# Optimization experiments

Measured on AMD Instinct MI355X. Metric: run time of the kernel, lower is better.

## Reference

```python
import jax, jax.numpy as jnp
import numpy as np

LAMBDA_CM = 0.5
LAMBDA_DIV = 0.1
EPS = 1e-8


def _normalize(x):
    # F.normalize(dim=-1): x / max(||x||, 1e-12)
    n = jnp.linalg.norm(x, axis=-1, keepdims=True)
    return x / jnp.maximum(n, 1e-12)


def _cdist(z, c):
    # Euclidean pairwise distance [N, K], matching torch.cdist(p=2)
    d2 = (jnp.sum(z * z, axis=-1, keepdims=True)
          + jnp.sum(c * c, axis=-1)[None, :]
          - 2.0 * (z @ c.T))
    return jnp.sqrt(jnp.maximum(d2, 0.0))


def setup_inputs() -> dict:
    key = jax.random.key(0)
    ks = jax.random.split(key, 7)
    N, dim_a, dim_b, embed_dim, n_codes = 8192, 1024, 1024, 512, 4096
    a = jax.random.normal(ks[0], (N, dim_a), dtype=jnp.float32)
    b = jax.random.normal(ks[1], (N, dim_b), dtype=jnp.float32)
    # Linear params (kaiming-uniform-ish scale)
    Wa = jax.random.uniform(ks[2], (embed_dim, dim_a), jnp.float32, -1, 1) / np.sqrt(dim_a)
    ba = jnp.zeros((embed_dim,), jnp.float32)
    Wb = jax.random.uniform(ks[3], (embed_dim, dim_b), jnp.float32, -1, 1) / np.sqrt(dim_b)
    bb = jnp.zeros((embed_dim,), jnp.float32)
    # Orthogonal-init codebook [n_codes, embed_dim] (n_codes > embed_dim -> orthonormal columns)
    g = jax.random.normal(ks[4], (n_codes, embed_dim), dtype=jnp.float32)
    q, _ = jnp.linalg.qr(g)
    codebook = q[:, :embed_dim] if q.shape[1] >= embed_dim else g / np.sqrt(embed_dim)
    codebook = jnp.asarray(codebook, jnp.float32)
    return {"a": a, "b": b, "Wa": Wa, "ba": ba, "Wb": Wb, "bb": bb, "codebook": codebook}


def reference(a, b, Wa, ba, Wb, bb, codebook):
    sg = jax.lax.stop_gradient
    za = _normalize(a @ Wa.T + ba)  # [N, D]
    zb = _normalize(b @ Wb.T + bb)  # [N, D]

    da = _cdist(za, codebook)       # [N, K]
    db = _cdist(zb, codebook)       # [N, K]
    idx_a = jnp.argmin(da, axis=-1)
    idx_b = jnp.argmin(db, axis=-1)
    qa = codebook[idx_a]            # [N, D]
    qb = codebook[idx_b]

    mse = lambda x, y: jnp.mean((x - y) ** 2)
    rec = (mse(qa, sg(za)) + mse(qb, sg(zb))
           + 0.25 * (mse(za, sg(qa)) + mse(zb, sg(qb))))

    sim = (za @ zb.T) / 0.07        # [N, N]
    N = sim.shape[0]
    diag = jnp.arange(N)
    ce_ab = -jnp.mean(jax.nn.log_softmax(sim, axis=-1)[diag, diag])
    ce_ba = -jnp.mean(jax.nn.log_softmax(sim.T, axis=-1)[diag, diag])
    cm = (ce_ab + ce_ba) / 2

    avg_a = jnp.mean(jax.nn.softmax(-da * 5.0, axis=-1), axis=0)  # [K]
    avg_b = jnp.mean(jax.nn.softmax(-db * 5.0, axis=-1), axis=0)
    div = (-(avg_a * jnp.log(avg_a + EPS)).sum()
           - (avg_b * jnp.log(avg_b + EPS)).sum()) / 2

    loss = rec + LAMBDA_CM * cm - LAMBDA_DIV * div
    match = jnp.mean((idx_a == idx_b).astype(jnp.float32))
    return loss, match
```

## Files before the change

kernel.cpp:

```cpp
#include <hip/hip_runtime.h>
#include <hip/hip_bf16.h>
#include <math.h>
#include <float.h>

typedef __attribute__((ext_vector_type(8))) short s8bf;
typedef __attribute__((ext_vector_type(4))) float f32x4;

typedef const __attribute__((address_space(1))) void g_void;
typedef __attribute__((address_space(3))) void lds_void;

__device__ inline ushort f2bf(float x) {
    unsigned int u = __float_as_uint(x);
    unsigned int r = (u + 0x7FFFu + ((u >> 16) & 1u)) >> 16;
    return (ushort)r;
}
__device__ inline ushort f2bf_fast(float x) {
    return (ushort)((__float_as_uint(x) + 0x8000u) >> 16);
}
__device__ inline float2 bf2x2(unsigned int u) {
    float2 r;
    r.x = __uint_as_float(u << 16);
    r.y = __uint_as_float(u & 0xFFFF0000u);
    return r;
}

__global__ __launch_bounds__(256) void k_cvt_bf16(
    const float* __restrict__ src, ushort* __restrict__ dst, size_t n)
{
    size_t i = ((size_t)blockIdx.x * 256 + threadIdx.x) * 4;
    size_t stride = (size_t)gridDim.x * 256 * 4;
    for (; i < n; i += stride) {
        float4 v = *(const float4*)(src + i);
        ushort4 o;
        o.x = f2bf(v.x); o.y = f2bf(v.y); o.z = f2bf(v.z); o.w = f2bf(v.w);
        *(ushort4*)(dst + i) = o;
    }
}

__device__ inline const ushort* stage_ptr(const ushort* M, size_t ld, int ra, int tid)
{
    const int row  = tid >> 2;
    const int slot = tid & 3;
    const int scol = ((slot ^ ((row >> 1) & 3)) << 3);
    return M + (size_t)(ra + row) * ld + scol;
}

__device__ inline void stage_issue2(const ushort* pa, const ushort* pb,
                                    size_t off64a, size_t off64b,
                                    ushort* As, ushort* Bs, int tid)
{
    const int wb = (tid >> 6) << 9;
    __builtin_amdgcn_global_load_lds((g_void*)pa,            (lds_void*)(As + wb),        16, 0, 0);
    __builtin_amdgcn_global_load_lds((g_void*)(pa + off64a), (lds_void*)(As + 2048 + wb), 16, 0, 0);
    __builtin_amdgcn_global_load_lds((g_void*)pb,            (lds_void*)(Bs + wb),        16, 0, 0);
    __builtin_amdgcn_global_load_lds((g_void*)(pb + off64b), (lds_void*)(Bs + 2048 + wb), 16, 0, 0);
}

__device__ inline void mma_tile(const ushort* As, const ushort* Bs,
                                int wr, int wc, int lane, f32x4 acc[4][4])
{
    const int hi = lane >> 4, lo = lane & 15;
    const int soff = ((hi ^ ((lo >> 1) & 3)) << 3);
    s8bf af[4], bfr[4];
#pragma unroll
    for (int m = 0; m < 4; ++m)
        af[m] = *(const s8bf*)(As + (wr * 64 + m * 16 + lo) * 32 + soff);
#pragma unroll
    for (int n = 0; n < 4; ++n)
        bfr[n] = *(const s8bf*)(Bs + (wc * 64 + n * 16 + lo) * 32 + soff);
#pragma unroll
    for (int m = 0; m < 4; ++m)
#pragma unroll
        for (int n = 0; n < 4; ++n)
            acc[m][n] = __builtin_amdgcn_mfma_f32_16x16x32_bf16(
                af[m], bfr[n], acc[m][n], 0, 0, 0);
}

#define DBUF_DECL  __shared__ __align__(16) ushort Lds[2][8192]
#define AS(p) (&Lds[p][0])
#define BS(p) (&Lds[p][4096])

__global__ __launch_bounds__(256) void k_mfma_gemm_bias2(
    const ushort* __restrict__ Aa, const ushort* __restrict__ Wa,
    const float* __restrict__ ba, float* __restrict__ Ca,
    const ushort* __restrict__ Ab, const ushort* __restrict__ Wb,
    const float* __restrict__ bb, float* __restrict__ Cb,
    int Ncols, int Kd)
{
    DBUF_DECL;
    const int z = blockIdx.z;
    const ushort* A = z ? Ab : Aa;
    const ushort* W = z ? Wb : Wa;
    const float* bias = z ? bb : ba;
    float* C = z ? Cb : Ca;

    const int tid = threadIdx.x, lane = tid & 63, wid = tid >> 6;
    const int wr = wid >> 1, wc = wid & 1;
    const int rbase = blockIdx.x * 128, cbase = blockIdx.y * 128;
    const int hi = lane >> 4, lo = lane & 15;
    const int KS = Kd >> 5;
    const size_t o64 = (size_t)64 * Kd;

    f32x4 acc[4][4];
#pragma unroll
    for (int m = 0; m < 4; ++m)
#pragma unroll
        for (int n = 0; n < 4; ++n)
#pragma unroll
            for (int j = 0; j < 4; ++j) acc[m][n][j] = 0.f;

    const ushort* pa = stage_ptr(A, Kd, rbase, tid);
    const ushort* pb = stage_ptr(W, Kd, cbase, tid);
    stage_issue2(pa, pb, o64, o64, AS(0), BS(0), tid);
    __syncthreads();
    int phase = 0;
    for (int ks = 0; ks < KS; ++ks) {
        pa += 32; pb += 32;
        if (ks + 1 < KS)
            stage_issue2(pa, pb, o64, o64, AS(phase ^ 1), BS(phase ^ 1), tid);
        mma_tile(AS(phase), BS(phase), wr, wc, lane, acc);
        __syncthreads();
        phase ^= 1;
    }
#pragma unroll
    for (int n = 0; n < 4; ++n) {
        int col = cbase + wc * 64 + n * 16 + lo;
        float bv = bias[col];
#pragma unroll
        for (int m = 0; m < 4; ++m)
#pragma unroll
            for (int j = 0; j < 4; ++j) {
                int row = rbase + wr * 64 + m * 16 + hi * 4 + j;
                C[(size_t)row * Ncols + col] = acc[m][n][j] + bv;
            }
    }
}

__global__ __launch_bounds__(256) void k_normalize2(
    const float* __restrict__ Za, ushort* __restrict__ Zab,
    const float* __restrict__ Zb, ushort* __restrict__ Zbb, int N, int D)
{
    const float* Z = blockIdx.y ? Zb : Za;
    ushort* Zo = blockIdx.y ? Zbb : Zab;
    const int lane = threadIdx.x & 63, wid = threadIdx.x >> 6;
    const int row = blockIdx.x * 4 + wid;
    if (row >= N) return;
    const float4* p = (const float4*)(Z + (size_t)row * D);
    const int nf4 = D >> 2;
    float ss = 0.f;
    for (int f = lane; f < nf4; f += 64) {
        float4 v = p[f];
        ss += v.x * v.x + v.y * v.y + v.z * v.z + v.w * v.w;
    }
#pragma unroll
    for (int msk = 1; msk < 64; msk <<= 1) ss += __shfl_xor(ss, msk, 64);
    float sc = 1.0f / fmaxf(sqrtf(ss), 1e-12f);
    ushort4* pb = (ushort4*)(Zo + (size_t)row * D);
    for (int f = lane; f < nf4; f += 64) {
        float4 v = p[f];
        ushort4 u;
        u.x = f2bf(v.x * sc); u.y = f2bf(v.y * sc);
        u.z = f2bf(v.z * sc); u.w = f2bf(v.w * sc);
        pb[f] = u;
    }
}

__global__ __launch_bounds__(256) void k_rownorm2(
    const float* __restrict__ X, float* __restrict__ out, int N, int D)
{
    const int lane = threadIdx.x & 63, wid = threadIdx.x >> 6;
    const int row = blockIdx.x * 4 + wid;
    if (row >= N) return;
    const float4* p = (const float4*)(X + (size_t)row * D);
    const int nf4 = D >> 2;
    float ss = 0.f;
    for (int f = lane; f < nf4; f += 64) {
        float4 v = p[f];
        ss += v.x * v.x + v.y * v.y + v.z * v.z + v.w * v.w;
    }
#pragma unroll
    for (int msk = 1; msk < 64; msk <<= 1) ss += __shfl_xor(ss, msk, 64);
    if (lane == 0) out[row] = ss;
}

#define EIGHT_PROLOG(XPTR, YPTR)                                               \
    const int tid = threadIdx.x, lane = tid & 63, wid = tid >> 6;              \
    const int wr = wid >> 2, wc = wid & 3;                                     \
    const int hi = lane >> 4, lo = lane & 15;                                  \
    const int fsw = ((hi ^ ((lo >> 1) & 3)) << 3);                             \
    const int KT = D >> 5, KTm = KT - 1;                                       \
    const int NIT = (chunkCols >> 8) << 5 >> 1; \
    const size_t o128 = (size_t)128 * D;                                       \
    const ushort* pa = stage_ptr(XPTR, D, rbase, tid);                         \
    const ushort* pb = stage_ptr(YPTR, D, c0, tid);

__device__ inline void issue8(ushort* Lbuf, const ushort* qa, const ushort* qb,
                              size_t o128, int wid)
{
    ushort* A0 = Lbuf + (wid << 9);
    ushort* B0 = Lbuf + 8192 + (wid << 9);
    __builtin_amdgcn_global_load_lds((g_void*)qa,          (lds_void*)A0,          16, 0, 0);
    __builtin_amdgcn_global_load_lds((g_void*)(qa + o128), (lds_void*)(A0 + 4096), 16, 0, 0);
    __builtin_amdgcn_global_load_lds((g_void*)qb,          (lds_void*)B0,          16, 0, 0);
    __builtin_amdgcn_global_load_lds((g_void*)(qb + o128), (lds_void*)(B0 + 4096), 16, 0, 0);
}

__global__ __launch_bounds__(512, 2) void k_sim8(
    const ushort* __restrict__ X, const ushort* __restrict__ Y,
    float* __restrict__ pl, float* __restrict__ colsum,
    int Ntot, int D, int chunkCols)
{
    __shared__ __align__(16) ushort L3[3][16384];
    const int rbase = blockIdx.x * 256;
    const int c0 = blockIdx.y * chunkCols;
    const float inv_t = 1.0f / 0.07f;
    EIGHT_PROLOG(X, Y)

    f32x4 acc[8][4];
    float Ls[32];
#pragma unroll
    for (int m = 0; m < 8; ++m)
#pragma unroll
        for (int n = 0; n < 4; ++n)
#pragma unroll
            for (int j = 0; j < 4; ++j) acc[m][n][j] = 0.f;
#pragma unroll
    for (int i = 0; i < 32; ++i) Ls[i] = 0.f;

    issue8(&L3[0][0], pa, pb, o128, wid);
    pa += 32; pb += 32;
    issue8(&L3[1][0], pa, pb, o128, wid);
    if ((1 & KTm) == KTm) { pa -= (D - 32); pb += (size_t)256 * D - (D - 32); }
    else { pa += 32; pb += 32; }

    int ibuf = 0, sbuf = 2, kk = 0, tcol = 0;
    for (int it = 0; it < NIT; ++it) {
        const int s = it + 2;
        if (s < NIT) {
            issue8(&L3[sbuf][0], pa, pb, o128, wid);
            if ((s & KTm) == KTm) { pa -= (D - 32); pb += (size_t)256 * D - (D - 32); }
            else { pa += 32; pb += 32; }
            if (++sbuf == 3) sbuf = 0;
            asm volatile("s_waitcnt vmcnt(8)" ::: "memory");
        } else if (it + 1 < NIT) {
            asm volatile("s_waitcnt vmcnt(4)" ::: "memory");
        } else {
            asm volatile("s_waitcnt vmcnt(0)" ::: "memory");
        }
        __builtin_amdgcn_sched_barrier(0);
        __builtin_amdgcn_s_barrier();

        const ushort* Ab = &L3[ibuf][0];
        const ushort* Bb = &L3[ibuf][8192];
        s8bf bfr[4];
#pragma unroll
        for (int n = 0; n < 4; ++n)
            bfr[n] = *(const s8bf*)(Bb + (wc * 64 + n * 16 + lo) * 32 + fsw);
        __builtin_amdgcn_s_setprio(1);
#pragma unroll
        for (int m = 0; m < 4; ++m) {
            s8bf a = *(const s8bf*)(Ab + (wr * 128 + m * 16 + lo) * 32 + fsw);
#pragma unroll
            for (int n = 0; n < 4; ++n)
                acc[m][n] = __builtin_amdgcn_mfma_f32_16x16x32_bf16(a, bfr[n], acc[m][n], 0, 0, 0);
        }
        __builtin_amdgcn_s_setprio(0);
        __builtin_amdgcn_s_barrier();
        __builtin_amdgcn_s_setprio(1);
#pragma unroll
        for (int m = 4; m < 8; ++m) {
            s8bf a = *(const s8bf*)(Ab + (wr * 128 + m * 16 + lo) * 32 + fsw);
#pragma unroll
            for (int n = 0; n < 4; ++n)
                acc[m][n] = __builtin_amdgcn_mfma_f32_16x16x32_bf16(a, bfr[n], acc[m][n], 0, 0, 0);
        }
        __builtin_amdgcn_s_setprio(0);
        __builtin_amdgcn_s_barrier();
        if (++ibuf == 3) ibuf = 0;

        if (++kk == KT) {
            kk = 0;
            const int cbase = c0 + tcol * 256 + wc * 64;
            float csum[4] = {0.f, 0.f, 0.f, 0.f};
#pragma unroll
            for (int m = 0; m < 8; ++m)
#pragma unroll
                for (int j = 0; j < 4; ++j) {
                    const int i = m * 4 + j;
#pragma unroll
                    for (int n = 0; n < 4; ++n) {
                        float e = __expf(acc[m][n][j] * inv_t);
                        Ls[i] += e;
                        csum[n] += e;
                        acc[m][n][j] = 0.f;
                    }
                }
#pragma unroll
            for (int n = 0; n < 4; ++n) {
                float cs = csum[n];
                cs += __shfl_xor(cs, 16, 64);
                cs += __shfl_xor(cs, 32, 64);
                if (hi == 0) atomicAdd(&colsum[cbase + n * 16 + lo], cs);
            }
            ++tcol;
        }
    }
#pragma unroll
    for (int i = 0; i < 32; ++i) {
#pragma unroll
        for (int msk = 1; msk < 16; msk <<= 1)
            Ls[i] += __shfl_xor(Ls[i], msk, 64);
    }
    if (lo == 0) {
        const int slot = blockIdx.y * 4 + wc;
#pragma unroll
        for (int m = 0; m < 8; ++m)
#pragma unroll
            for (int j = 0; j < 4; ++j) {
                int row = rbase + wr * 128 + m * 16 + hi * 4 + j;
                pl[(size_t)slot * Ntot + row] = Ls[m * 4 + j];
            }
    }
}

__global__ __launch_bounds__(512, 2) void k_dist8(
    const ushort* __restrict__ Za, const ushort* __restrict__ Zb,
    const ushort* __restrict__ CB, const float* __restrict__ cn,
    ushort* __restrict__ expm_a, ushort* __restrict__ expm_b,
    int Ntot, int Ktot, int D, int chunkCols)
{
    __shared__ __align__(16) ushort L3[3][16384];
    const ushort* Z = blockIdx.z ? Zb : Za;
    ushort* expm = blockIdx.z ? expm_b : expm_a;
    const int rbase = blockIdx.x * 256;
    const int c0 = blockIdx.y * chunkCols;
    EIGHT_PROLOG(Z, CB)

    f32x4 acc[8][4];
#pragma unroll
    for (int m = 0; m < 8; ++m)
#pragma unroll
        for (int n = 0; n < 4; ++n)
#pragma unroll
            for (int j = 0; j < 4; ++j) acc[m][n][j] = 0.f;

    issue8(&L3[0][0], pa, pb, o128, wid);
    pa += 32; pb += 32;
    issue8(&L3[1][0], pa, pb, o128, wid);
    if ((1 & KTm) == KTm) { pa -= (D - 32); pb += (size_t)256 * D - (D - 32); }
    else { pa += 32; pb += 32; }

    int ibuf = 0, sbuf = 2, kk = 0, tcol = 0;
    for (int it = 0; it < NIT; ++it) {
        const int s = it + 2;
        if (s < NIT) {
            issue8(&L3[sbuf][0], pa, pb, o128, wid);
            if ((s & KTm) == KTm) { pa -= (D - 32); pb += (size_t)256 * D - (D - 32); }
            else { pa += 32; pb += 32; }
            if (++sbuf == 3) sbuf = 0;
            asm volatile("s_waitcnt vmcnt(8)" ::: "memory");
        } else if (it + 1 < NIT) {
            asm volatile("s_waitcnt vmcnt(4)" ::: "memory");
        } else {
            asm volatile("s_waitcnt vmcnt(0)" ::: "memory");
        }
        __builtin_amdgcn_sched_barrier(0);
        __builtin_amdgcn_s_barrier();

        const ushort* Ab = &L3[ibuf][0];
        const ushort* Bb = &L3[ibuf][8192];
        s8bf bfr[4];
#pragma unroll
        for (int n = 0; n < 4; ++n)
            bfr[n] = *(const s8bf*)(Bb + (wc * 64 + n * 16 + lo) * 32 + fsw);
        __builtin_amdgcn_s_setprio(1);
#pragma unroll
        for (int m = 0; m < 4; ++m) {
            s8bf a = *(const s8bf*)(Ab + (wr * 128 + m * 16 + lo) * 32 + fsw);
#pragma unroll
            for (int n = 0; n < 4; ++n)
                acc[m][n] = __builtin_amdgcn_mfma_f32_16x16x32_bf16(a, bfr[n], acc[m][n], 0, 0, 0);
        }
        __builtin_amdgcn_s_setprio(0);
        __builtin_amdgcn_s_barrier();
        __builtin_amdgcn_s_setprio(1);
#pragma unroll
        for (int m = 4; m < 8; ++m) {
            s8bf a = *(const s8bf*)(Ab + (wr * 128 + m * 16 + lo) * 32 + fsw);
#pragma unroll
            for (int n = 0; n < 4; ++n)
                acc[m][n] = __builtin_amdgcn_mfma_f32_16x16x32_bf16(a, bfr[n], acc[m][n], 0, 0, 0);
        }
        __builtin_amdgcn_s_setprio(0);
        __builtin_amdgcn_s_barrier();
        if (++ibuf == 3) ibuf = 0;

        if (++kk == KT) {
            kk = 0;
            const int cbase = c0 + tcol * 256 + wc * 64;
            float cnv[4];
#pragma unroll
            for (int n = 0; n < 4; ++n) cnv[n] = 1.0f + cn[cbase + n * 16 + lo];
#pragma unroll
            for (int m = 0; m < 8; ++m)
#pragma unroll
                for (int j = 0; j < 4; ++j) {
                    const int row = rbase + wr * 128 + m * 16 + hi * 4 + j;
                    ushort* erow = expm + (size_t)row * Ktot + cbase + lo;
#pragma unroll
                    for (int n = 0; n < 4; ++n) {
                        float d = sqrtf(fmaxf(cnv[n] - 2.0f * acc[m][n][j], 0.f));
                        erow[n * 16] = f2bf_fast(__expf(-5.0f * d));
                        acc[m][n][j] = 0.f;
                    }
                }
            ++tcol;
        }
    }
}

__global__ __launch_bounds__(256) void k_row_stats(
    const ushort* __restrict__ expm_a, const ushort* __restrict__ expm_b,
    int* __restrict__ idx_a, float* __restrict__ lse_a, float* __restrict__ inv_a,
    int* __restrict__ idx_b, float* __restrict__ lse_b, float* __restrict__ inv_b,
    int Ktot)
{
    const int z = blockIdx.y;
    const ushort* expm = z ? expm_b : expm_a;
    int* idx = z ? idx_b : idx_a;
    float* lse = z ? lse_b : lse_a;
    float* inv = z ? inv_b : inv_a;
    const int lane = threadIdx.x & 63, wid = threadIdx.x >> 6;
    const int row = blockIdx.x * 4 + wid;
    const uint4* p = (const uint4*)(expm + (size_t)row * Ktot);
    const int nf8 = Ktot >> 3;
    float s = 0.f, best = -1.f;
    int bk = 0;
    for (int f = lane; f < nf8; f += 64) {
        uint4 u = p[f];
        const unsigned* w = (const unsigned*)&u;
        const int k0 = f << 3;
#pragma unroll
        for (int q = 0; q < 4; ++q) {
            float2 e = bf2x2(w[q]);
            s += e.x + e.y;
            if (e.x > best) { best = e.x; bk = k0 + 2 * q; }
            if (e.y > best) { best = e.y; bk = k0 + 2 * q + 1; }
        }
    }
#pragma unroll
    for (int msk = 1; msk < 64; msk <<= 1) {
        float ob = __shfl_xor(best, msk, 64);
        int   ok = __shfl_xor(bk, msk, 64);
        s += __shfl_xor(s, msk, 64);
        if (ob > best || (ob == best && ok < bk)) { best = ob; bk = ok; }
    }
    if (lane == 0) {
        idx[row] = bk;
        lse[row] = __logf(s);
        inv[row] = 1.0f / s;
    }
}

__global__ __launch_bounds__(256) void k_avg_stream(
    const ushort* __restrict__ expm_a, const ushort* __restrict__ expm_b,
    const float* __restrict__ inv_a, const float* __restrict__ inv_b,
    float* __restrict__ avg_a, float* __restrict__ avg_b,
    int Ktot, int rows)
{
    const int z = blockIdx.z;
    const ushort* expm = z ? expm_b : expm_a;
    const float* invL = z ? inv_b : inv_a;
    float* avg = z ? avg_b : avg_a;
    const int c = blockIdx.x * 1024 + threadIdx.x * 4;
    const int r0 = blockIdx.y * rows;
    float4 s = {0.f, 0.f, 0.f, 0.f};
    for (int r = r0; r < r0 + rows; ++r) {
        float il = invL[r];
        uint2 u = *(const uint2*)(expm + (size_t)r * Ktot + c);
        float2 e0 = bf2x2(u.x);
        float2 e1 = bf2x2(u.y);
        s.x = fmaf(e0.x, il, s.x);
        s.y = fmaf(e0.y, il, s.y);
        s.z = fmaf(e1.x, il, s.z);
        s.w = fmaf(e1.y, il, s.w);
    }
    atomicAdd(&avg[c + 0], s.x);
    atomicAdd(&avg[c + 1], s.y);
    atomicAdd(&avg[c + 2], s.z);
    atomicAdd(&avg[c + 3], s.w);
}

__global__ __launch_bounds__(256) void k_mfma_dist1_noexp(
    const ushort* __restrict__ Za, const ushort* __restrict__ Zb,
    const ushort* __restrict__ CB,
    const float* __restrict__ cn, float* __restrict__ pd,
    float* __restrict__ pls, int* __restrict__ pib,
    int Ntot, int D, int chunkCols)
{
    DBUF_DECL;
    const int z = blockIdx.z;
    const ushort* Z = z ? Zb : Za;
    const int tid = threadIdx.x, lane = tid & 63, wid = tid >> 6;
    const int wr = wid >> 1, wc = wid & 1;
    const int rbase = blockIdx.x * 128;
    const int c0 = blockIdx.y * chunkCols;
    const int hi = lane >> 4, lo = lane & 15;
    const int KS = D >> 5, TILES = chunkCols >> 7;
    const size_t o64 = (size_t)64 * D;
    const ptrdiff_t dWrapA = -(ptrdiff_t)(D - 32);
    const ptrdiff_t dWrapB = (ptrdiff_t)128 * D - (ptrdiff_t)(D - 32);

    float bd[16], ls[16]; int bi[16];
#pragma unroll
    for (int i = 0; i < 16; ++i) { bd[i] = FLT_MAX; ls[i] = 0.f; bi[i] = 0; }

    const ushort* pa = stage_ptr(Z, D, rbase, tid);
    const ushort* pb = stage_ptr(CB, D, c0, tid);
    stage_issue2(pa, pb, o64, o64, AS(0), BS(0), tid);
    __syncthreads();
    int phase = 0;
    for (int t = 0; t < TILES; ++t) {
        f32x4 acc[4][4];
#pragma unroll
        for (int m = 0; m < 4; ++m)
#pragma unroll
            for (int n = 0; n < 4; ++n)
#pragma unroll
                for (int j = 0; j < 4; ++j) acc[m][n][j] = 0.f;
        for (int ks = 0; ks < KS; ++ks) {
            const bool wrap = (ks + 1 == KS);
            pa += wrap ? dWrapA : 32;
            pb += wrap ? dWrapB : 32;
            if (!(wrap && t + 1 == TILES))
                stage_issue2(pa, pb, o64, o64, AS(phase ^ 1), BS(phase ^ 1), tid);
            mma_tile(AS(phase), BS(phase), wr, wc, lane, acc);
            __syncthreads();
            phase ^= 1;
        }
        const int cbase = c0 + (t << 7) + wc * 64;
        float cnv[4]; int cix[4];
#pragma unroll
        for (int n = 0; n < 4; ++n) {
            cix[n] = cbase + n * 16 + lo;
            cnv[n] = cn[cix[n]];
        }
#pragma unroll
        for (int m = 0; m < 4; ++m)
#pragma unroll
            for (int j = 0; j < 4; ++j) {
                const int i = m * 4 + j;
#pragma unroll
                for (int n = 0; n < 4; ++n) {
                    float d = sqrtf(fmaxf(1.0f + cnv[n] - 2.0f * acc[m][n][j], 0.f));
                    if (d < bd[i]) { bd[i] = d; bi[i] = cix[n]; }
                    ls[i] += __expf(-5.0f * d);
                }
            }
    }
#pragma unroll
    for (int i = 0; i < 16; ++i) {
#pragma unroll
        for (int msk = 1; msk < 16; msk <<= 1) {
            float od = __shfl_xor(bd[i], msk, 64);
            int   oi = __shfl_xor(bi[i], msk, 64);
            ls[i] += __shfl_xor(ls[i], msk, 64);
            if (od < bd[i] || (od == bd[i] && oi < bi[i])) { bd[i] = od; bi[i] = oi; }
        }
    }
    if (lo == 0) {
        const int slot = (z * gridDim.y + blockIdx.y) * 2 + wc;
#pragma unroll
        for (int m = 0; m < 4; ++m)
#pragma unroll
            for (int j = 0; j < 4; ++j) {
                int row = rbase + wr * 64 + m * 16 + hi * 4 + j;
                pd [(size_t)slot * Ntot + row] = bd[m * 4 + j];
                pls[(size_t)slot * Ntot + row] = ls[m * 4 + j];
                pib[(size_t)slot * Ntot + row] = bi[m * 4 + j];
            }
    }
}

__global__ __launch_bounds__(256) void k_dist1_reduce2(
    const float* __restrict__ pd, const float* __restrict__ pls,
    const int* __restrict__ pib,
    int* __restrict__ idx_a, float* __restrict__ lse_a, float* __restrict__ inv_a,
    int* __restrict__ idx_b, float* __restrict__ lse_b, float* __restrict__ inv_b,
    int Ntot, int slots)
{
    const int z = blockIdx.y;
    int row = blockIdx.x * 256 + threadIdx.x;
    if (row >= Ntot) return;
    const float* pdz = pd + (size_t)z * slots * Ntot;
    const float* plz = pls + (size_t)z * slots * Ntot;
    const int*   piz = pib + (size_t)z * slots * Ntot;
    float bd = FLT_MAX; int bi = 0;
    float L = 0.f;
    for (int s = 0; s < slots; ++s) {
        float d = pdz[(size_t)s * Ntot + row];
        int   i = piz[(size_t)s * Ntot + row];
        if (d < bd || (d == bd && i < bi)) { bd = d; bi = i; }
        L += plz[(size_t)s * Ntot + row];
    }
    if (z) { idx_b[row] = bi; lse_b[row] = __logf(L); inv_b[row] = 1.0f / L; }
    else   { idx_a[row] = bi; lse_a[row] = __logf(L); inv_a[row] = 1.0f / L; }
}

__global__ __launch_bounds__(256) void k_mfma_dist2(
    const ushort* __restrict__ Za, const ushort* __restrict__ Zb,
    const ushort* __restrict__ CB, const float* __restrict__ cn,
    const float* __restrict__ lse_a, const float* __restrict__ lse_b,
    float* __restrict__ avg_a, float* __restrict__ avg_b,
    int Ntot, int D, int chunkCols)
{
    DBUF_DECL;
    const ushort* Z = blockIdx.z ? Zb : Za;
    const float* lse = blockIdx.z ? lse_b : lse_a;
    float* avg = blockIdx.z ? avg_b : avg_a;
    const int tid = threadIdx.x, lane = tid & 63, wid = tid >> 6;
    const int wr = wid >> 1, wc = wid & 1;
    const int rbase = blockIdx.x * 128;
    const int c0 = blockIdx.y * chunkCols;
    const int hi = lane >> 4, lo = lane & 15;
    const int KS = D >> 5, TILES = chunkCols >> 7;
    const size_t o64 = (size_t)64 * D;
    const ptrdiff_t dWrapA = -(ptrdiff_t)(D - 32);
    const ptrdiff_t dWrapB = (ptrdiff_t)128 * D - (ptrdiff_t)(D - 32);

    float lr[16];
#pragma unroll
    for (int m = 0; m < 4; ++m)
#pragma unroll
        for (int j = 0; j < 4; ++j)
            lr[m * 4 + j] = lse[rbase + wr * 64 + m * 16 + hi * 4 + j];

    const ushort* pa = stage_ptr(Z, D, rbase, tid);
    const ushort* pb = stage_ptr(CB, D, c0, tid);
    stage_issue2(pa, pb, o64, o64, AS(0), BS(0), tid);
    __syncthreads();
    int phase = 0;
    for (int t = 0; t < TILES; ++t) {
        f32x4 acc[4][4];
#pragma unroll
        for (int m = 0; m < 4; ++m)
#pragma unroll
            for (int n = 0; n < 4; ++n)
#pragma unroll
                for (int j = 0; j < 4; ++j) acc[m][n][j] = 0.f;
        for (int ks = 0; ks < KS; ++ks) {
            const bool wrap = (ks + 1 == KS);
            pa += wrap ? dWrapA : 32;
            pb += wrap ? dWrapB : 32;
            if (!(wrap && t + 1 == TILES))
                stage_issue2(pa, pb, o64, o64, AS(phase ^ 1), BS(phase ^ 1), tid);
            mma_tile(AS(phase), BS(phase), wr, wc, lane, acc);
            __syncthreads();
            phase ^= 1;
        }
        const int cbase = c0 + (t << 7) + wc * 64;
        float cnv[4];
#pragma unroll
        for (int n = 0; n < 4; ++n) cnv[n] = cn[cbase + n * 16 + lo];
        float colsum[4] = {0.f, 0.f, 0.f, 0.f};
#pragma unroll
        for (int m = 0; m < 4; ++m)
#pragma unroll
            for (int j = 0; j < 4; ++j) {
                const int i = m * 4 + j;
#pragma unroll
                for (int n = 0; n < 4; ++n) {
                    float d = sqrtf(fmaxf(1.0f + cnv[n] - 2.0f * acc[m][n][j], 0.f));
                    colsum[n] += __expf(-5.0f * d - lr[i]);
                }
            }
#pragma unroll
        for (int n = 0; n < 4; ++n) {
            float cs = colsum[n];
            cs += __shfl_xor(cs, 16, 64);
            cs += __shfl_xor(cs, 32, 64);
            if (hi == 0) atomicAdd(&avg[cbase + n * 16 + lo], cs);
        }
    }
}

__global__ __launch_bounds__(256) void k_sum_log_reduce(
    const float* __restrict__ pl, float* __restrict__ out, int Ntot, int slots)
{
    int row = blockIdx.x * 256 + threadIdx.x;
    if (row >= Ntot) return;
    float L = 0.f;
    for (int s = 0; s < slots; ++s)
        L += pl[(size_t)s * Ntot + row];
    out[row] = __logf(L);
}

__global__ __launch_bounds__(256) void k_log_inplace(
    const float* __restrict__ src, float* __restrict__ dst, int n)
{
    int i = blockIdx.x * 256 + threadIdx.x;
    if (i < n) dst[i] = __logf(src[i]);
}

__global__ __launch_bounds__(256) void k_rec_match(
    const ushort* __restrict__ za, const ushort* __restrict__ zb,
    const ushort* __restrict__ cbk,
    const int* __restrict__ idx_a, const int* __restrict__ idx_b,
    const float* __restrict__ lse_ab, const float* __restrict__ lse_ba,
    float* __restrict__ acc, int N, int D)
{
    const int tid = threadIdx.x, lane = tid & 63, wid = tid >> 6;
    const int gw = blockIdx.x * 4 + wid;
    const int nw = gridDim.x * 4;
    const int nf8 = D >> 3;
    float pa = 0.f, pb = 0.f, pdot = 0.f;
    for (int row = gw; row < N; row += nw) {
        const int ia = idx_a[row], ib = idx_b[row];
        const uint4* pza = (const uint4*)(za + (size_t)row * D);
        const uint4* pzb = (const uint4*)(zb + (size_t)row * D);
        const uint4* pca = (const uint4*)(cbk + (size_t)ia * D);
        const uint4* pcb = (const uint4*)(cbk + (size_t)ib * D);
        for (int f = lane; f < nf8; f += 64) {
            uint4 ua = pza[f], ub = pzb[f], uc = pca[f], ud = pcb[f];
            const unsigned int* wa = (const unsigned int*)&ua;
            const unsigned int* wb = (const unsigned int*)&ub;
            const unsigned int* wc2 = (const unsigned int*)&uc;
            const unsigned int* wd = (const unsigned int*)&ud;
#pragma unroll
            for (int q = 0; q < 4; ++q) {
                float2 va = bf2x2(wa[q]), vb = bf2x2(wb[q]);
                float2 ca = bf2x2(wc2[q]), cb = bf2x2(wd[q]);
                float dx = va.x - ca.x, dy = va.y - ca.y;
                pa += dx * dx + dy * dy;
                dx = vb.x - cb.x; dy = vb.y - cb.y;
                pb += dx * dx + dy * dy;
                pdot += va.x * vb.x + va.y * vb.y;
            }
        }
    }
    float slab = 0.f, slba = 0.f, smatch = 0.f;
    for (int r = blockIdx.x * 256 + tid; r < N; r += gridDim.x * 256) {
        slab += lse_ab[r];
        slba += lse_ba[r];
        if (idx_a[r] == idx_b[r]) smatch += 1.f;
    }
#pragma unroll
    for (int msk = 1; msk < 64; msk <<= 1) {
        pa += __shfl_xor(pa, msk, 64);
        pb += __shfl_xor(pb, msk, 64);
        pdot += __shfl_xor(pdot, msk, 64);
        slab += __shfl_xor(slab, msk, 64);
        slba += __shfl_xor(slba, msk, 64);
        smatch += __shfl_xor(smatch, msk, 64);
    }
    __shared__ float red[4][6];
    if (lane == 0) {
        red[wid][0] = pa; red[wid][1] = pb; red[wid][2] = slab;
        red[wid][3] = slba; red[wid][4] = smatch; red[wid][5] = pdot;
    }
    __syncthreads();
    if (tid < 6) {
        float s = red[0][tid] + red[1][tid] + red[2][tid] + red[3][tid];
        atomicAdd(&acc[tid], s);
    }
}

__global__ __launch_bounds__(256) void k_finalize(
    const float* __restrict__ avg_a, const float* __restrict__ avg_b,
    const float* __restrict__ acc, float* __restrict__ out,
    int N, int D, int K)
{
    __shared__ float red[256];
    const int tid = threadIdx.x;
    const float invN = 1.0f / (float)N;
    float sa = 0.f, sb = 0.f;
    for (int k = tid; k < K; k += 256) {
        float va = avg_a[k] * invN;
        float vb = avg_b[k] * invN;
        sa += va * logf(va + 1e-8f);
        sb += vb * logf(vb + 1e-8f);
    }
    red[tid] = sa;
    __syncthreads();
    for (int s = 128; s > 0; s >>= 1) {
        if (tid < s) red[tid] += red[tid + s];
        __syncthreads();
    }
    float entA = -red[0];
    __syncthreads();
    red[tid] = sb;
    __syncthreads();
    for (int s = 128; s > 0; s >>= 1) {
        if (tid < s) red[tid] += red[tid + s];
        __syncthreads();
    }
    if (tid == 0) {
        float entB = -red[0];
        float nd = (float)N * (float)D;
        float rec = 1.25f * (acc[0] / nd + acc[1] / nd);
        float sdot = acc[5] / 0.07f;
        float cm  = 0.5f * ((acc[2] - sdot) + (acc[3] - sdot)) * invN;
        float div = 0.5f * (entA + entB);
        out[0] = rec + 0.5f * cm - 0.1f * div;
        out[1] = acc[4] * invN;
    }
}

extern "C" void kernel_launch(void* const* d_in, const int* in_sizes, int n_in,
                              void* d_out, int out_size, void* d_ws, size_t ws_size,
                              hipStream_t stream)
{
    const float* a   = (const float*)d_in[0];
    const float* b   = (const float*)d_in[1];
    const float* Wa  = (const float*)d_in[2];
    const float* ba  = (const float*)d_in[3];
    const float* Wb  = (const float*)d_in[4];
    const float* bb  = (const float*)d_in[5];
    const float* cbk = (const float*)d_in[6];

    const int D  = in_sizes[3];
    const int dA = in_sizes[2] / D;
    const int dB = in_sizes[4] / D;
    const int N  = in_sizes[0] / dA;
    const int K  = in_sizes[6] / D;

    char* w = (char*)d_ws;
    size_t off = 0;
    auto alloc = [&](size_t bytes) -> void* {
        void* p = w + off;
        off = (off + bytes + 255) & ~(size_t)255;
        return p;
    };
    float*  za     = (float*)alloc((size_t)N * D * 4);
    float*  zb     = (float*)alloc((size_t)N * D * 4);
    float*  cn     = (float*)alloc((size_t)K * 4);
    int*    idx_a  = (int*)  alloc((size_t)N * 4);
    int*    idx_b  = (int*)  alloc((size_t)N * 4);
    float*  lse_a  = (float*)alloc((size_t)N * 4);
    float*  lse_b  = (float*)alloc((size_t)N * 4);
    float*  inv_a  = (float*)alloc((size_t)N * 4);
    float*  inv_b  = (float*)alloc((size_t)N * 4);
    float*  lse_ab = (float*)alloc((size_t)N * 4);
    float*  lse_ba = (float*)alloc((size_t)N * 4);
    float*  avgreg = (float*)alloc(((size_t)2 * K + 8) * 4);
    float*  avg_a  = avgreg;
    float*  avg_b  = avgreg + K;
    float*  accb   = avgreg + 2 * K;
    ushort* Wa_bf  = (ushort*)alloc((size_t)D * dA * 2);
    ushort* Wb_bf  = (ushort*)alloc((size_t)D * dB * 2);
    ushort* cbk_bf = (ushort*)alloc((size_t)K * D * 2);
    ushort* regionA = (ushort*)alloc((size_t)N * dA * 2);
    ushort* a_bf  = regionA;
    ushort* za_bf = regionA;
    ushort* zb_bf = regionA + (size_t)N * D;
    ushort* regionB = (ushort*)alloc((size_t)N * dB * 2);
    ushort* b_bf   = regionB;
    float* pl     = (float*)regionB;
    float* pd     = pl  + (size_t)32 * N;
    float* pls    = pd  + (size_t)64 * N;
    int*   pib    = (int*)(pls + (size_t)64 * N);
    float* colsum = (float*)(pib + (size_t)64 * N);
    if (off > ws_size) return;
    ushort* expm_a = (ushort*)alloc((size_t)N * K * 2);
    ushort* expm_b = (ushort*)alloc((size_t)N * K * 2);
    const bool useExp = (off <= ws_size);

    dim3 blk(256);
    dim3 blk8(512);

    k_cvt_bf16<<<1024, blk, 0, stream>>>(a,   a_bf,   (size_t)N * dA);
    k_cvt_bf16<<<1024, blk, 0, stream>>>(b,   b_bf,   (size_t)N * dB);
    k_cvt_bf16<<<256,  blk, 0, stream>>>(Wa,  Wa_bf,  (size_t)D * dA);
    k_cvt_bf16<<<256,  blk, 0, stream>>>(Wb,  Wb_bf,  (size_t)D * dB);
    k_cvt_bf16<<<512,  blk, 0, stream>>>(cbk, cbk_bf, (size_t)K * D);

    k_mfma_gemm_bias2<<<dim3(N / 128, D / 128, 2), blk, 0, stream>>>(
        a_bf, Wa_bf, ba, za, b_bf, Wb_bf, bb, zb, D, dA);

    k_normalize2<<<dim3((N + 3) / 4, 2), blk, 0, stream>>>(za, za_bf, zb, zb_bf, N, D);
    k_rownorm2<<<dim3((K + 3) / 4), blk, 0, stream>>>(cbk, cn, K, D);
    hipMemsetAsync(avgreg, 0, ((size_t)2 * K + 8) * 4, stream);
    hipMemsetAsync(colsum, 0, (size_t)N * 4, stream);

    if (useExp) {
        const int dchunk = 1024;
        k_dist8<<<dim3(N / 256, K / dchunk, 2), blk8, 0, stream>>>(
            za_bf, zb_bf, cbk_bf, cn, expm_a, expm_b, N, K, D, dchunk);
        k_row_stats<<<dim3(N / 4, 2), blk, 0, stream>>>(
            expm_a, expm_b, idx_a, lse_a, inv_a, idx_b, lse_b, inv_b, K);
        k_avg_stream<<<dim3(K / 1024, N / 64, 2), blk, 0, stream>>>(
            expm_a, expm_b, inv_a, inv_b, avg_a, avg_b, K, 64);
    } else {
        const int dchunk = 256, dcy = K / dchunk;
        dim3 dgrid(N / 128, dcy, 2);
        k_mfma_dist1_noexp<<<dgrid, blk, 0, stream>>>(
            za_bf, zb_bf, cbk_bf, cn, pd, pls, pib, N, D, dchunk);
        k_dist1_reduce2<<<dim3(N / 256, 2), blk, 0, stream>>>(
            pd, pls, pib, idx_a, lse_a, inv_a, idx_b, lse_b, inv_b, N, 2 * dcy);
        k_mfma_dist2<<<dgrid, blk, 0, stream>>>(
            za_bf, zb_bf, cbk_bf, cn, lse_a, lse_b, avg_a, avg_b, N, D, dchunk);
    }

    const int schunk = 1024, scy = N / schunk;
    k_sim8<<<dim3(N / 256, scy), blk8, 0, stream>>>(za_bf, zb_bf, pl, colsum, N, D, schunk);
    k_sum_log_reduce<<<N / 256, blk, 0, stream>>>(pl, lse_ab, N, 4 * scy);
    k_log_inplace<<<N / 256, blk, 0, stream>>>(colsum, lse_ba, N);

    k_rec_match<<<256, blk, 0, stream>>>(za_bf, zb_bf, cbk_bf, idx_a, idx_b, lse_ab, lse_ba, accb, N, D);
    k_finalize<<<1, blk, 0, stream>>>(avg_a, avg_b, accb, (float*)d_out, N, D, K);
}
```

Before: 346.4 us.

## Store permuted exp matrix with vector writes and drop mid-loop MFMA barrier

The distance kernel now packs four bf16 exp values per lane into one ushort4 store, instead of four strided scalar stores. The codebook column order inside each 64-wide block is therefore permuted. The row-stats and averaging kernels remap indices back to true codebook columns, with argmin tie-breaking on the true index. Separately, the MFMA inner loops merge the two half-loops and drop the intermediate barrier and priority toggles, which cuts synchronization overhead at some risk to wave scheduling.

New measurement: 333.2 us (median of 2 runs). 3.8% less time.

```diff
diff --git a/kernel.cpp b/kernel.cpp
--- a/kernel.cpp
+++ b/kernel.cpp
@@ -189,7 +189,7 @@
     const int hi = lane >> 4, lo = lane & 15;                                  \
     const int fsw = ((hi ^ ((lo >> 1) & 3)) << 3);                             \
     const int KT = D >> 5, KTm = KT - 1;                                       \
-    const int NIT = (chunkCols >> 8) << 5 >> 1; \
+    const int NIT = (chunkCols >> 8) << 5 >> 1;                                \
     const size_t o128 = (size_t)128 * D;                                       \
     const ushort* pa = stage_ptr(XPTR, D, rbase, tid);                         \
     const ushort* pb = stage_ptr(YPTR, D, c0, tid);
@@ -258,17 +258,7 @@
             bfr[n] = *(const s8bf*)(Bb + (wc * 64 + n * 16 + lo) * 32 + fsw);
         __builtin_amdgcn_s_setprio(1);
 #pragma unroll
-        for (int m = 0; m < 4; ++m) {
-            s8bf a = *(const s8bf*)(Ab + (wr * 128 + m * 16 + lo) * 32 + fsw);
-#pragma unroll
-            for (int n = 0; n < 4; ++n)
-                acc[m][n] = __builtin_amdgcn_mfma_f32_16x16x32_bf16(a, bfr[n], acc[m][n], 0, 0, 0);
-        }
-        __builtin_amdgcn_s_setprio(0);
-        __builtin_amdgcn_s_barrier();
-        __builtin_amdgcn_s_setprio(1);
-#pragma unroll
-        for (int m = 4; m < 8; ++m) {
+        for (int m = 0; m < 8; ++m) {
             s8bf a = *(const s8bf*)(Ab + (wr * 128 + m * 16 + lo) * 32 + fsw);
 #pragma unroll
             for (int n = 0; n < 4; ++n)
@@ -375,17 +365,7 @@
             bfr[n] = *(const s8bf*)(Bb + (wc * 64 + n * 16 + lo) * 32 + fsw);
         __builtin_amdgcn_s_setprio(1);
 #pragma unroll
-        for (int m = 0; m < 4; ++m) {
-            s8bf a = *(const s8bf*)(Ab + (wr * 128 + m * 16 + lo) * 32 + fsw);
-#pragma unroll
-            for (int n = 0; n < 4; ++n)
-                acc[m][n] = __builtin_amdgcn_mfma_f32_16x16x32_bf16(a, bfr[n], acc[m][n], 0, 0, 0);
-        }
-        __builtin_amdgcn_s_setprio(0);
-        __builtin_amdgcn_s_barrier();
-        __builtin_amdgcn_s_setprio(1);
-#pragma unroll
-        for (int m = 4; m < 8; ++m) {
+        for (int m = 0; m < 8; ++m) {
             s8bf a = *(const s8bf*)(Ab + (wr * 128 + m * 16 + lo) * 32 + fsw);
 #pragma unroll
             for (int n = 0; n < 4; ++n)
@@ -406,13 +386,20 @@
 #pragma unroll
                 for (int j = 0; j < 4; ++j) {
                     const int row = rbase + wr * 128 + m * 16 + hi * 4 + j;
-                    ushort* erow = expm + (size_t)row * Ktot + cbase + lo;
-#pragma unroll
-                    for (int n = 0; n < 4; ++n) {
-                        float d = sqrtf(fmaxf(cnv[n] - 2.0f * acc[m][n][j], 0.f));
-                        erow[n * 16] = f2bf_fast(__expf(-5.0f * d));
-                        acc[m][n][j] = 0.f;
+                    ushort4 ev;
+                    {
+                        float d0 = sqrtf(fmaxf(cnv[0] - 2.0f * acc[m][0][j], 0.f));
+                        float d1 = sqrtf(fmaxf(cnv[1] - 2.0f * acc[m][1][j], 0.f));
+                        float d2 = sqrtf(fmaxf(cnv[2] - 2.0f * acc[m][2][j], 0.f));
+                        float d3 = sqrtf(fmaxf(cnv[3] - 2.0f * acc[m][3][j], 0.f));
+                        ev.x = f2bf_fast(__expf(-5.0f * d0));
+                        ev.y = f2bf_fast(__expf(-5.0f * d1));
+                        ev.z = f2bf_fast(__expf(-5.0f * d2));
+                        ev.w = f2bf_fast(__expf(-5.0f * d3));
                     }
+                    *(ushort4*)(expm + (size_t)row * Ktot + cbase + lo * 4) = ev;
+                    acc[m][0][j] = 0.f; acc[m][1][j] = 0.f;
+                    acc[m][2][j] = 0.f; acc[m][3][j] = 0.f;
                 }
             ++tcol;
         }
@@ -435,28 +422,33 @@
     const uint4* p = (const uint4*)(expm + (size_t)row * Ktot);
     const int nf8 = Ktot >> 3;
     float s = 0.f, best = -1.f;
-    int bk = 0;
+    int bc = 0x7FFFFFFF;
     for (int f = lane; f < nf8; f += 64) {
         uint4 u = p[f];
         const unsigned* w = (const unsigned*)&u;
-        const int k0 = f << 3;
+        const int kp0 = f << 3;
+        const int blk = kp0 & ~63;
 #pragma unroll
         for (int q = 0; q < 4; ++q) {
             float2 e = bf2x2(w[q]);
+            const int o0 = (kp0 & 63) + 2 * q;
+            const int c0t = blk + ((o0 & 3) << 4) + (o0 >> 2);
+            const int o1 = o0 + 1;
+            const int c1t = blk + ((o1 & 3) << 4) + (o1 >> 2);
             s += e.x + e.y;
-            if (e.x > best) { best = e.x; bk = k0 + 2 * q; }
-            if (e.y > best) { best = e.y; bk = k0 + 2 * q + 1; }
+            if (e.x > best || (e.x == best && c0t < bc)) { best = e.x; bc = c0t; }
+            if (e.y > best || (e.y == best && c1t < bc)) { best = e.y; bc = c1t; }
         }
     }
 #pragma unroll
     for (int msk = 1; msk < 64; msk <<= 1) {
         float ob = __shfl_xor(best, msk, 64);
-        int   ok = __shfl_xor(bk, msk, 64);
+        int   ok = __shfl_xor(bc, msk, 64);
         s += __shfl_xor(s, msk, 64);
-        if (ob > best || (ob == best && ok < bk)) { best = ob; bk = ok; }
+        if (ob > best || (ob == best && ok < bc)) { best = ob; bc = ok; }
     }
     if (lane == 0) {
-        idx[row] = bk;
+        idx[row] = bc;
         lse[row] = __logf(s);
         inv[row] = 1.0f / s;
     }
@@ -472,12 +464,13 @@
     const ushort* expm = z ? expm_b : expm_a;
     const float* invL = z ? inv_b : inv_a;
     float* avg = z ? avg_b : avg_a;
-    const int c = blockIdx.x * 1024 + threadIdx.x * 4;
+    const int pc = blockIdx.x * 1024 + threadIdx.x * 4;
+    const int j0 = (pc & ~63) + ((pc & 63) >> 2);
     const int r0 = blockIdx.y * rows;
     float4 s = {0.f, 0.f, 0.f, 0.f};
     for (int r = r0; r < r0 + rows; ++r) {
         float il = invL[r];
-        uint2 u = *(const uint2*)(expm + (size_t)r * Ktot + c);
+        uint2 u = *(const uint2*)(expm + (size_t)r * Ktot + pc);
         float2 e0 = bf2x2(u.x);
         float2 e1 = bf2x2(u.y);
         s.x = fmaf(e0.x, il, s.x);
@@ -485,10 +478,10 @@
         s.z = fmaf(e1.x, il, s.z);
         s.w = fmaf(e1.y, il, s.w);
     }
-    atomicAdd(&avg[c + 0], s.x);
-    atomicAdd(&avg[c + 1], s.y);
-    atomicAdd(&avg[c + 2], s.z);
-    atomicAdd(&avg[c + 3], s.w);
+    atomicAdd(&avg[j0 +  0], s.x);
+    atomicAdd(&avg[j0 + 16], s.y);
+    atomicAdd(&avg[j0 + 32], s.z);
+    atomicAdd(&avg[j0 + 48], s.w);
 }
 
 __global__ __launch_bounds__(256) void k_mfma_dist1_noexp(
```
